# Optimization experiments

Measured on AMD Instinct MI355X. Metric: run time of the kernel, lower is better.

The kernel has to match this reference:

```python
import jax, jax.numpy as jnp
import numpy as np

ATTN_HEADS = 4
NEG_INF = float(np.finfo(np.float32).min)


def setup_inputs() -> dict:
    key = jax.random.key(0)
    ks = jax.random.split(key, 7)
    B, N, K, Cin, Cout = 4, 4096, 32, 128, 128
    h_X = jax.random.normal(ks[0], (B, N, Cout), dtype=jnp.float32)
    h_E = jax.random.normal(ks[1], (B, N, K, Cin), dtype=jnp.float32)
    mask_attn = jax.random.randint(ks[2], (B, N, K), 0, 2, dtype=jnp.int32)
    # torch Linear weights are [out_features, in_features]
    W_Q = jax.random.normal(ks[3], (Cout, Cout), dtype=jnp.float32) / np.sqrt(Cout)
    W_K = jax.random.normal(ks[4], (Cout, Cin), dtype=jnp.float32) / np.sqrt(Cin)
    W_V = jax.random.normal(ks[5], (Cout, Cin), dtype=jnp.float32) / np.sqrt(Cin)
    W_O = jax.random.normal(ks[6], (Cout, 3 * Cout), dtype=jnp.float32) / np.sqrt(3 * Cout)
    return {"h_X": h_X, "h_E": h_E, "mask_attn": mask_attn,
            "W_Q": W_Q, "W_K": W_K, "W_V": W_V, "W_O": W_O}


def reference(h_X, h_E, mask_attn, W_Q, W_K, W_V, W_O):
    B, N, K, _ = h_E.shape
    C = W_Q.shape[0]
    H = ATTN_HEADS
    d = C // H

    h_q = (h_X @ W_Q.T).reshape(B, N, H, d)          # [B,N,H,d]
    h_k = (h_E @ W_K.T).reshape(B, N, K, H, d)       # [B,N,K,H,d]
    h_v = (h_E @ W_V.T).reshape(B, N, K, H, d)       # [B,N,K,H,d]

    # per-node, per-head scores over K neighbors
    scores = jnp.einsum('bnhd,bnkhd->bnhk', h_q, h_k) / np.sqrt(d)

    mask = (mask_attn[:, :, None, :] > 0)            # [B,N,1,K] -> broadcast over heads
    logits = jnp.where(mask, scores, NEG_INF)
    attn = jax.nn.softmax(logits, axis=-1) * mask.astype(scores.dtype)  # [B,N,H,K]

    attn_sum = attn.sum(axis=-1, keepdims=True) + 1e-8                  # [B,N,H,1]
    hv_t = jnp.swapaxes(h_v, 2, 3)                                      # [B,N,H,K,d]
    weighted_v = attn[..., None] * hv_t                                 # [B,N,H,K,d]
    weighted_sum = weighted_v.sum(axis=3)                               # [B,N,H,d]
    aggr_mean = (weighted_sum / attn_sum).reshape(B, N, C)
    aggr_sum = weighted_sum.reshape(B, N, C)
    aggr_max = weighted_v.max(axis=3).reshape(B, N, C)

    aggr_cat = jnp.concatenate([aggr_mean, aggr_sum, aggr_max], axis=-1)  # [B,N,3C]
    return aggr_cat @ W_O.T                                               # [B,N,C]
```

## Files before the change

kernel.cpp:

```cpp
#include <hip/hip_runtime.h>
#include <stdint.h>


typedef __attribute__((ext_vector_type(8))) short short8;
typedef __attribute__((ext_vector_type(4))) float f32x4;

#define CDIM  128
#define KN    32
#define ESTR  136
#define SSTR  36

__device__ __forceinline__ float bf2f(short s) {
    union { unsigned int u; float f; } v;
    v.u = ((unsigned int)(unsigned short)s) << 16;
    return v.f;
}
__device__ __forceinline__ short f2bf(float f) {
    union { float ff; unsigned int u; } v; v.ff = f;
    unsigned int u = v.u;
    u += 0x7FFFu + ((u >> 16) & 1u);
    return (short)(u >> 16);
}

template<bool FP32>
__device__ __forceinline__ short8 load8bf(const void* p, size_t idx) {
    if constexpr (FP32) {
        const float* fp = (const float*)p + idx;
        f32x4 a = *(const f32x4*)fp;
        f32x4 b = *(const f32x4*)(fp + 4);
        short8 r;
        r[0] = f2bf(a[0]); r[1] = f2bf(a[1]); r[2] = f2bf(a[2]); r[3] = f2bf(a[3]);
        r[4] = f2bf(b[0]); r[5] = f2bf(b[1]); r[6] = f2bf(b[2]); r[7] = f2bf(b[3]);
        return r;
    } else {
        return *(const short8*)((const short*)p + idx);
    }
}

template<bool FP32>
__device__ __forceinline__ short loadbf1(const void* p, size_t idx) {
    if constexpr (FP32) return f2bf(((const float*)p)[idx]);
    else return ((const short*)p)[idx];
}

__device__ __forceinline__ bool detect_fp32(const short* wp) {
    const int lane = threadIdx.x & 63;
    int cnt = 0;
    #pragma unroll
    for (int i = 0; i < 8; ++i) {
        const float v = bf2f(wp[lane + i * 64]);
        if (!(fabsf(v) < 8.0f)) cnt++;
    }
    #pragma unroll
    for (int d = 1; d < 64; d <<= 1) cnt += __shfl_xor(cnt, d);
    return cnt > 16;
}

#define ANPB 64
struct alignas(16) SmemA {
    short sX[ANPB * ESTR];
    short sQ[ANPB * ESTR];
};

template<bool FP32>
__device__ __forceinline__ void naA_body(SmemA& sm, const void* __restrict__ hX,
    const void* __restrict__ WQ, const void* __restrict__ WK, short* __restrict__ Tg)
{
    const int tid = threadIdx.x, lane = tid & 63, w = tid >> 6;
    const int quad = lane >> 4, l15 = lane & 15;
    const int nbA = blockIdx.x * ANPB;

    #pragma unroll
    for (int it = 0; it < 4; ++it) {
        const int chunk = it * 256 + tid, row = chunk >> 4, cc = chunk & 15;
        *(short8*)&sm.sX[row * ESTR + cc * 8] =
            load8bf<FP32>(hX, (size_t)nbA * CDIM + (size_t)chunk * 8);
    }
    short8 bq[2][4];
    #pragma unroll
    for (int t2 = 0; t2 < 2; ++t2)
        #pragma unroll
        for (int kk = 0; kk < 4; ++kk)
            bq[t2][kk] = load8bf<FP32>(WQ, (size_t)(w * 32 + t2 * 16 + l15) * CDIM + kk * 32 + quad * 8);
    __syncthreads();

    #pragma unroll
    for (int mt = 0; mt < 4; ++mt) {
        short8 ax[4];
        #pragma unroll
        for (int kk = 0; kk < 4; ++kk)
            ax[kk] = *(const short8*)&sm.sX[(mt * 16 + l15) * ESTR + kk * 32 + quad * 8];
        f32x4 o0 = {0.f,0.f,0.f,0.f}, o1 = {0.f,0.f,0.f,0.f};
        #pragma unroll
        for (int kk = 0; kk < 4; ++kk) {
            o0 = __builtin_amdgcn_mfma_f32_16x16x32_bf16(ax[kk], bq[0][kk], o0, 0, 0, 0);
            o1 = __builtin_amdgcn_mfma_f32_16x16x32_bf16(ax[kk], bq[1][kk], o1, 0, 0, 0);
        }
        #pragma unroll
        for (int r = 0; r < 4; ++r) {
            const int row = mt * 16 + quad * 4 + r;
            sm.sQ[row * ESTR + w * 32 + l15]      = f2bf(o0[r]);
            sm.sQ[row * ESTR + w * 32 + 16 + l15] = f2bf(o1[r]);
        }
    }
    __syncthreads();

    short8 bk[2][4];
    #pragma unroll
    for (int t2 = 0; t2 < 2; ++t2)
        #pragma unroll
        for (int kk = 0; kk < 4; ++kk) {
            const int j = w * 32 + t2 * 16 + l15;
            short8 b;
            #pragma unroll
            for (int jj = 0; jj < 8; ++jj)
                b[jj] = loadbf1<FP32>(WK, (size_t)(kk * 32 + quad * 8 + jj) * CDIM + j);
            bk[t2][kk] = b;
        }

    const float scale = 0.17677669529663687f;
    const short8 zz = {0,0,0,0,0,0,0,0};
    #pragma unroll
    for (int m = 0; m < 16; ++m) {
        const int n_g = (m * 16 + l15) >> 2, h_ = l15 & 3;
        const short8 qv = *(const short8*)&sm.sQ[n_g * ESTR + h_ * 32 + quad * 8];
        f32x4 c0 = {0.f,0.f,0.f,0.f}, c1 = {0.f,0.f,0.f,0.f};
        #pragma unroll
        for (int kk = 0; kk < 4; ++kk) {
            const short8 af = (kk == h_) ? qv : zz;
            c0 = __builtin_amdgcn_mfma_f32_16x16x32_bf16(af, bk[0][kk], c0, 0, 0, 0);
            c1 = __builtin_amdgcn_mfma_f32_16x16x32_bf16(af, bk[1][kk], c1, 0, 0, 0);
        }
        #pragma unroll
        for (int r = 0; r < 4; ++r) {
            const int rg = m * 16 + quad * 4 + r;
            const size_t base = (size_t)(nbA + (rg >> 2)) * 512 + (rg & 3) * 128 + w * 32;
            Tg[base + l15]      = f2bf(c0[r] * scale);
            Tg[base + 16 + l15] = f2bf(c1[r] * scale);
        }
    }
}

__global__ __launch_bounds__(256, 3)
void naA(const void* __restrict__ hX, const void* __restrict__ WQ,
         const void* __restrict__ WK, short* __restrict__ Tg)
{
    __shared__ SmemA sm;
    if (detect_fp32((const short*)WQ)) naA_body<true >(sm, hX, WQ, WK, Tg);
    else                               naA_body<false>(sm, hX, WQ, WK, Tg);
}

#define NPB 16
struct alignas(16) SmemB {
    short sE[128 * ESTR];
    short sTb[2][16 * ESTR];
    float sS[16 * SSTR];
    int   sMask[NPB * KN];
};

template<bool FP32>
__device__ __forceinline__ void issueE(const void* hE, size_t base, int tid,
                                       f32x4 (&eF)[8][2], short8 (&eB)[8]) {
    if constexpr (FP32) {
        #pragma unroll
        for (int it = 0; it < 8; ++it) {
            const float* p = (const float*)hE + base + (size_t)(it * 256 + tid) * 8;
            eF[it][0] = *(const f32x4*)p;
            eF[it][1] = *(const f32x4*)(p + 4);
        }
    } else {
        #pragma unroll
        for (int it = 0; it < 8; ++it)
            eB[it] = *(const short8*)((const short*)hE + base + (size_t)(it * 256 + tid) * 8);
    }
}

template<bool FP32>
__device__ __forceinline__ void writeE(short* sE, int tid,
                                       const f32x4 (&eF)[8][2], const short8 (&eB)[8]) {
    #pragma unroll
    for (int it = 0; it < 8; ++it) {
        const int chunk = it * 256 + tid, row = chunk >> 4, cc = chunk & 15;
        short8 v;
        if constexpr (FP32) {
            #pragma unroll
            for (int t = 0; t < 4; ++t) { v[t] = f2bf(eF[it][0][t]); v[4 + t] = f2bf(eF[it][1][t]); }
        } else v = eB[it];
        *(short8*)&sE[row * ESTR + cc * 8] = v;
    }
}

template<bool FP32>
__device__ __forceinline__ void naB_body(SmemB& sm, const void* __restrict__ hE,
    const int* __restrict__ mask, const void* __restrict__ WV,
    const short* __restrict__ Tg, short* __restrict__ catG)
{
    const int tid = threadIdx.x, lane = tid & 63, w = tid >> 6;
    const int quad = lane >> 4, l15 = lane & 15;
    const int nb = blockIdx.x * NPB;
    const size_t ebase = (size_t)nb * (KN * CDIM);

    f32x4 eF[8][2]; short8 eB[8]; short8 eT;
    issueE<FP32>(hE, ebase, tid, eF, eB);
    eT = *(const short8*)(Tg + (size_t)nb * 512 + tid * 8);
    __builtin_amdgcn_sched_barrier(0);

    *(int2*)&sm.sMask[tid * 2] = *(const int2*)&mask[(size_t)nb * KN + tid * 2];

    short8 bv[2][4];
    #pragma unroll
    for (int ct2 = 0; ct2 < 2; ++ct2)
        #pragma unroll
        for (int kk = 0; kk < 4; ++kk)
            bv[ct2][kk] = load8bf<FP32>(WV, (size_t)((2 * w + ct2) * 16 + l15) * CDIM + kk * 32 + quad * 8);

    writeE<FP32>(sm.sE, tid, eF, eB);
    { const int row = tid >> 4, cc = tid & 15;
      *(short8*)&sm.sTb[0][row * ESTR + cc * 8] = eT; }
    issueE<FP32>(hE, ebase + 128 * 128, tid, eF, eB);
    eT = *(const short8*)(Tg + (size_t)(nb + 4) * 512 + tid * 8);
    __builtin_amdgcn_sched_barrier(0);
    __syncthreads();

    #pragma unroll 1
    for (int s = 0; s < 4; ++s) {
        const short* tb = sm.sTb[s & 1];

        short8 bs[4], a0[4], a1[4];
        #pragma unroll
        for (int kk = 0; kk < 4; ++kk) {
            bs[kk] = *(const short8*)&tb[l15 * ESTR + kk * 32 + quad * 8];
            a0[kk] = *(const short8*)&sm.sE[(w * 32 + l15) * ESTR + kk * 32 + quad * 8];
            a1[kk] = *(const short8*)&sm.sE[(w * 32 + 16 + l15) * ESTR + kk * 32 + quad * 8];
        }
        f32x4 s0 = {0.f,0.f,0.f,0.f}, s1 = {0.f,0.f,0.f,0.f};
        #pragma unroll
        for (int kk = 0; kk < 4; ++kk) {
            s0 = __builtin_amdgcn_mfma_f32_16x16x32_bf16(a0[kk], bs[kk], s0, 0, 0, 0);
            s1 = __builtin_amdgcn_mfma_f32_16x16x32_bf16(a1[kk], bs[kk], s1, 0, 0, 0);
        }

        {
            const int* mp = &sm.sMask[(s * 4 + (l15 >> 2)) * KN];
            float x[8]; int mk[8];
            #pragma unroll
            for (int j = 0; j < 4; ++j) {
                x[j] = s0[j];     mk[j]     = mp[quad * 4 + j];
                x[4 + j] = s1[j]; mk[4 + j] = mp[16 + quad * 4 + j];
            }
            float m = -3.0e38f;
            #pragma unroll
            for (int j = 0; j < 8; ++j) m = fmaxf(m, (mk[j] > 0) ? x[j] : -3.0e38f);
            m = fmaxf(m, __shfl_xor(m, 16));
            m = fmaxf(m, __shfl_xor(m, 32));
            float dsum = 0.f;
            #pragma unroll
            for (int j = 0; j < 8; ++j) {
                const float e = __expf(fminf(x[j] - m, 0.f)) * ((mk[j] > 0) ? 1.f : 0.f);
                x[j] = e; dsum += e;
            }
            dsum += __shfl_xor(dsum, 16);
            dsum += __shfl_xor(dsum, 32);
            const float inv = (dsum > 0.f) ? (1.f / dsum) : 0.f;
            if ((l15 >> 2) == w) {
                float* sp = &sm.sS[(w * 4 + (l15 & 3)) * SSTR];
                #pragma unroll
                for (int j = 0; j < 4; ++j) {
                    sp[quad * 4 + j]      = x[j] * inv;
                    sp[16 + quad * 4 + j] = x[4 + j] * inv;
                }
                if (quad == 0)
                    sp[33] = 1.0f / (((dsum > 0.f) ? 1.0f : 0.0f) + 1e-8f);
            }
        }
        __syncthreads();

        #pragma unroll
        for (int n_ = 0; n_ < 4; ++n_) {
            short8 c0[4], c1[4];
            #pragma unroll
            for (int kk = 0; kk < 4; ++kk) {
                c0[kk] = *(const short8*)&sm.sE[(n_ * 32 + l15) * ESTR + kk * 32 + quad * 8];
                c1[kk] = *(const short8*)&sm.sE[(n_ * 32 + 16 + l15) * ESTR + kk * 32 + quad * 8];
            }
            const float* ap = &sm.sS[(n_ * 4 + w) * SSTR];
            const float ainv = ap[33];
            #pragma unroll
            for (int ct2 = 0; ct2 < 2; ++ct2) {
                f32x4 av0 = {0.f,0.f,0.f,0.f}, av1 = {0.f,0.f,0.f,0.f};
                #pragma unroll
                for (int kk = 0; kk < 4; ++kk) {
                    av0 = __builtin_amdgcn_mfma_f32_16x16x32_bf16(c0[kk], bv[ct2][kk], av0, 0, 0, 0);
                    av1 = __builtin_amdgcn_mfma_f32_16x16x32_bf16(c1[kk], bv[ct2][kk], av1, 0, 0, 0);
                }
                float sum = 0.f, mx = -3.0e38f;
                #pragma unroll
                for (int r = 0; r < 4; ++r) {
                    const float p0 = ap[quad * 4 + r]      * av0[r];
                    const float p1 = ap[16 + quad * 4 + r] * av1[r];
                    sum += p0 + p1;
                    mx = fmaxf(mx, fmaxf(p0, p1));
                }
                sum += __shfl_xor(sum, 16);
                sum += __shfl_xor(sum, 32);
                mx = fmaxf(mx, __shfl_xor(mx, 16));
                mx = fmaxf(mx, __shfl_xor(mx, 32));
                if (quad == 0) {
                    const int c = (2 * w + ct2) * 16 + l15;
                    const size_t ng = (size_t)(nb + s * 4 + n_) * 384;
                    catG[ng + c]       = f2bf(sum * ainv);
                    catG[ng + 128 + c] = f2bf(sum);
                    catG[ng + 256 + c] = f2bf(mx);
                }
            }
        }
        __syncthreads();

        if (s < 3) {
            writeE<FP32>(sm.sE, tid, eF, eB);
            { const int row = tid >> 4, cc = tid & 15;
              *(short8*)&sm.sTb[(s + 1) & 1][row * ESTR + cc * 8] = eT; }
            if (s < 2) {
                issueE<FP32>(hE, ebase + (size_t)(s + 2) * 128 * 128, tid, eF, eB);
                eT = *(const short8*)(Tg + (size_t)(nb + (s + 2) * 4) * 512 + tid * 8);
                __builtin_amdgcn_sched_barrier(0);
            }
            __syncthreads();
        }
    }
}

__global__ __launch_bounds__(256, 3)
void naB(const void* __restrict__ hE, const int* __restrict__ mask,
         const void* __restrict__ WV, const short* __restrict__ Tg,
         short* __restrict__ catG)
{
    __shared__ SmemB sm;
    if (detect_fp32((const short*)WV)) naB_body<true >(sm, hE, mask, WV, Tg, catG);
    else                               naB_body<false>(sm, hE, mask, WV, Tg, catG);
}

struct alignas(16) SmemC {
    short sCat[16 * 392];
};

template<bool FP32>
__device__ __forceinline__ void naC_body(SmemC& sm, const short* __restrict__ catG,
    const void* __restrict__ WO, void* __restrict__ out)
{
    const int tid = threadIdx.x, lane = tid & 63, w = tid >> 6;
    const int quad = lane >> 4, l15 = lane & 15;
    const int nb = blockIdx.x * 16;

    #pragma unroll
    for (int it = 0; it < 3; ++it) {
        const int chunk = it * 256 + tid;
        const int row = chunk / 48, cc = chunk % 48;
        *(short8*)&sm.sCat[row * 392 + cc * 8] =
            *(const short8*)&catG[(size_t)nb * 384 + (size_t)chunk * 8];
    }
    __syncthreads();

    f32x4 o0 = {0.f,0.f,0.f,0.f}, o1 = {0.f,0.f,0.f,0.f};
    #pragma unroll
    for (int kk = 0; kk < 12; ++kk) {
        const short8 a  = *(const short8*)&sm.sCat[l15 * 392 + kk * 32 + quad * 8];
        const short8 b0 = load8bf<FP32>(WO, (size_t)(w * 32 + l15) * 384 + kk * 32 + quad * 8);
        const short8 b1 = load8bf<FP32>(WO, (size_t)(w * 32 + 16 + l15) * 384 + kk * 32 + quad * 8);
        o0 = __builtin_amdgcn_mfma_f32_16x16x32_bf16(a, b0, o0, 0, 0, 0);
        o1 = __builtin_amdgcn_mfma_f32_16x16x32_bf16(a, b1, o1, 0, 0, 0);
    }
    #pragma unroll
    for (int r = 0; r < 4; ++r) {
        const int node = quad * 4 + r;
        const size_t base = (size_t)(nb + node) * CDIM + w * 32;
        if constexpr (FP32) {
            ((float*)out)[base + l15]      = o0[r];
            ((float*)out)[base + 16 + l15] = o1[r];
        } else {
            ((short*)out)[base + l15]      = f2bf(o0[r]);
            ((short*)out)[base + 16 + l15] = f2bf(o1[r]);
        }
    }
}

__global__ __launch_bounds__(256, 4)
void naC(const short* __restrict__ catG, const void* __restrict__ WO,
         void* __restrict__ out)
{
    __shared__ SmemC sm;
    if (detect_fp32((const short*)WO)) naC_body<true >(sm, catG, WO, out);
    else                               naC_body<false>(sm, catG, WO, out);
}

extern "C" void kernel_launch(void* const* d_in, const int* in_sizes, int n_in,
                              void* d_out, int out_size, void* d_ws, size_t ws_size,
                              hipStream_t stream) {
    (void)in_sizes; (void)n_in; (void)ws_size; (void)out_size;
    const void* hX   = d_in[0];
    const void* hE   = d_in[1];
    const int*  mask = (const int*)d_in[2];
    const void* WQ   = d_in[3];
    const void* WK   = d_in[4];
    const void* WV   = d_in[5];
    const void* WO   = d_in[6];

    short* Tg   = (short*)d_ws;
    short* catG = (short*)((char*)d_ws + (32u << 20));

    naA<<<dim3(256),  dim3(256), 0, stream>>>(hX, WQ, WK, Tg);
    naB<<<dim3(1024), dim3(256), 0, stream>>>(hE, mask, WV, Tg, catG);
    naC<<<dim3(1024), dim3(256), 0, stream>>>(catG, WO, d_out);
}
```

Before: 434.0 us.

## Restructure attention kernel to one node per wavefront without shared memory

Result: slower. 494.6 us (+14.0%).

```diff
diff --git a/kernel.cpp b/kernel.cpp
--- a/kernel.cpp
+++ b/kernel.cpp
@@ -8,7 +8,7 @@
 #define CDIM  128
 #define KN    32
 #define ESTR  136
-#define SSTR  36
+#define NEGI  -3.0e38f
 
 __device__ __forceinline__ float bf2f(short s) {
     union { unsigned int u; float f; } v;
@@ -150,194 +150,114 @@
     else                               naA_body<false>(sm, hX, WQ, WK, Tg);
 }
 
-#define NPB 16
-struct alignas(16) SmemB {
-    short sE[128 * ESTR];
-    short sTb[2][16 * ESTR];
-    float sS[16 * SSTR];
-    int   sMask[NPB * KN];
-};
-
-template<bool FP32>
-__device__ __forceinline__ void issueE(const void* hE, size_t base, int tid,
-                                       f32x4 (&eF)[8][2], short8 (&eB)[8]) {
-    if constexpr (FP32) {
-        #pragma unroll
-        for (int it = 0; it < 8; ++it) {
-            const float* p = (const float*)hE + base + (size_t)(it * 256 + tid) * 8;
-            eF[it][0] = *(const f32x4*)p;
-            eF[it][1] = *(const f32x4*)(p + 4);
-        }
-    } else {
-        #pragma unroll
-        for (int it = 0; it < 8; ++it)
-            eB[it] = *(const short8*)((const short*)hE + base + (size_t)(it * 256 + tid) * 8);
-    }
-}
-
-template<bool FP32>
-__device__ __forceinline__ void writeE(short* sE, int tid,
-                                       const f32x4 (&eF)[8][2], const short8 (&eB)[8]) {
-    #pragma unroll
-    for (int it = 0; it < 8; ++it) {
-        const int chunk = it * 256 + tid, row = chunk >> 4, cc = chunk & 15;
-        short8 v;
-        if constexpr (FP32) {
-            #pragma unroll
-            for (int t = 0; t < 4; ++t) { v[t] = f2bf(eF[it][0][t]); v[4 + t] = f2bf(eF[it][1][t]); }
-        } else v = eB[it];
-        *(short8*)&sE[row * ESTR + cc * 8] = v;
-    }
-}
-
-template<bool FP32>
-__device__ __forceinline__ void naB_body(SmemB& sm, const void* __restrict__ hE,
+template<bool FP32>
+__device__ __forceinline__ void naB2_node(int node, const void* __restrict__ hE,
     const int* __restrict__ mask, const void* __restrict__ WV,
     const short* __restrict__ Tg, short* __restrict__ catG)
 {
-    const int tid = threadIdx.x, lane = tid & 63, w = tid >> 6;
+    const int lane = threadIdx.x & 63;
     const int quad = lane >> 4, l15 = lane & 15;
-    const int nb = blockIdx.x * NPB;
-    const size_t ebase = (size_t)nb * (KN * CDIM);
-
-    f32x4 eF[8][2]; short8 eB[8]; short8 eT;
-    issueE<FP32>(hE, ebase, tid, eF, eB);
-    eT = *(const short8*)(Tg + (size_t)nb * 512 + tid * 8);
-    __builtin_amdgcn_sched_barrier(0);
-
-    *(int2*)&sm.sMask[tid * 2] = *(const int2*)&mask[(size_t)nb * KN + tid * 2];
-
-    short8 bv[2][4];
-    #pragma unroll
-    for (int ct2 = 0; ct2 < 2; ++ct2)
-        #pragma unroll
-        for (int kk = 0; kk < 4; ++kk)
-            bv[ct2][kk] = load8bf<FP32>(WV, (size_t)((2 * w + ct2) * 16 + l15) * CDIM + kk * 32 + quad * 8);
-
-    writeE<FP32>(sm.sE, tid, eF, eB);
-    { const int row = tid >> 4, cc = tid & 15;
-      *(short8*)&sm.sTb[0][row * ESTR + cc * 8] = eT; }
-    issueE<FP32>(hE, ebase + 128 * 128, tid, eF, eB);
-    eT = *(const short8*)(Tg + (size_t)(nb + 4) * 512 + tid * 8);
-    __builtin_amdgcn_sched_barrier(0);
-    __syncthreads();
-
-    #pragma unroll 1
-    for (int s = 0; s < 4; ++s) {
-        const short* tb = sm.sTb[s & 1];
-
-        short8 bs[4], a0[4], a1[4];
+    const size_t eb = (size_t)node * (KN * CDIM);
+
+    short8 aE0[4], aE1[4];
+    #pragma unroll
+    for (int kk = 0; kk < 4; ++kk) {
+        aE0[kk] = load8bf<FP32>(hE, eb + (size_t)l15 * CDIM + kk * 32 + quad * 8);
+        aE1[kk] = load8bf<FP32>(hE, eb + (size_t)(16 + l15) * CDIM + kk * 32 + quad * 8);
+    }
+
+    short8 tq[4];
+    #pragma unroll
+    for (int kk = 0; kk < 4; ++kk)
+        tq[kk] = *(const short8*)(Tg + (size_t)node * 512 + (l15 & 3) * 128 + kk * 32 + quad * 8);
+
+    const int mk0 = mask[(size_t)node * KN + l15];
+    const int mk1 = mask[(size_t)node * KN + 16 + l15];
+
+    f32x4 s0 = {0.f,0.f,0.f,0.f}, s1 = {0.f,0.f,0.f,0.f};
+    #pragma unroll
+    for (int kk = 0; kk < 4; ++kk) {
+        s0 = __builtin_amdgcn_mfma_f32_16x16x32_bf16(tq[kk], aE0[kk], s0, 0, 0, 0);
+        s1 = __builtin_amdgcn_mfma_f32_16x16x32_bf16(tq[kk], aE1[kk], s1, 0, 0, 0);
+    }
+
+    float x0[4], x1[4], ainv[4];
+    {
+        float m[4], ds[4];
+        #pragma unroll
+        for (int r = 0; r < 4; ++r) {
+            const float a = (mk0 > 0) ? s0[r] : NEGI;
+            const float b = (mk1 > 0) ? s1[r] : NEGI;
+            m[r] = fmaxf(a, b);
+        }
+        #pragma unroll
+        for (int d = 1; d < 16; d <<= 1)
+            #pragma unroll
+            for (int r = 0; r < 4; ++r) m[r] = fmaxf(m[r], __shfl_xor(m[r], d));
+        #pragma unroll
+        for (int r = 0; r < 4; ++r) {
+            x0[r] = __expf(fminf(s0[r] - m[r], 0.f)) * ((mk0 > 0) ? 1.f : 0.f);
+            x1[r] = __expf(fminf(s1[r] - m[r], 0.f)) * ((mk1 > 0) ? 1.f : 0.f);
+            ds[r] = x0[r] + x1[r];
+        }
+        #pragma unroll
+        for (int d = 1; d < 16; d <<= 1)
+            #pragma unroll
+            for (int r = 0; r < 4; ++r) ds[r] += __shfl_xor(ds[r], d);
+        #pragma unroll
+        for (int r = 0; r < 4; ++r) {
+            const float inv = (ds[r] > 0.f) ? (1.f / ds[r]) : 0.f;
+            x0[r] *= inv; x1[r] *= inv;
+            ainv[r] = 1.0f / (((ds[r] > 0.f) ? 1.0f : 0.0f) + 1e-8f);
+        }
+    }
+
+    const size_t ng = (size_t)node * 384;
+    #pragma unroll
+    for (int ct = 0; ct < 8; ++ct) {
+        const int h = ct >> 1;
+        float aA[4], aB[4];
+        #pragma unroll
+        for (int r = 0; r < 4; ++r) {
+            aA[r] = __shfl(x0[h], quad * 4 + r);
+            aB[r] = __shfl(x1[h], quad * 4 + r);
+        }
+        f32x4 av0 = {0.f,0.f,0.f,0.f}, av1 = {0.f,0.f,0.f,0.f};
         #pragma unroll
         for (int kk = 0; kk < 4; ++kk) {
-            bs[kk] = *(const short8*)&tb[l15 * ESTR + kk * 32 + quad * 8];
-            a0[kk] = *(const short8*)&sm.sE[(w * 32 + l15) * ESTR + kk * 32 + quad * 8];
-            a1[kk] = *(const short8*)&sm.sE[(w * 32 + 16 + l15) * ESTR + kk * 32 + quad * 8];
-        }
-        f32x4 s0 = {0.f,0.f,0.f,0.f}, s1 = {0.f,0.f,0.f,0.f};
-        #pragma unroll
-        for (int kk = 0; kk < 4; ++kk) {
-            s0 = __builtin_amdgcn_mfma_f32_16x16x32_bf16(a0[kk], bs[kk], s0, 0, 0, 0);
-            s1 = __builtin_amdgcn_mfma_f32_16x16x32_bf16(a1[kk], bs[kk], s1, 0, 0, 0);
-        }
-
-        {
-            const int* mp = &sm.sMask[(s * 4 + (l15 >> 2)) * KN];
-            float x[8]; int mk[8];
-            #pragma unroll
-            for (int j = 0; j < 4; ++j) {
-                x[j] = s0[j];     mk[j]     = mp[quad * 4 + j];
-                x[4 + j] = s1[j]; mk[4 + j] = mp[16 + quad * 4 + j];
-            }
-            float m = -3.0e38f;
-            #pragma unroll
-            for (int j = 0; j < 8; ++j) m = fmaxf(m, (mk[j] > 0) ? x[j] : -3.0e38f);
-            m = fmaxf(m, __shfl_xor(m, 16));
-            m = fmaxf(m, __shfl_xor(m, 32));
-            float dsum = 0.f;
-            #pragma unroll
-            for (int j = 0; j < 8; ++j) {
-                const float e = __expf(fminf(x[j] - m, 0.f)) * ((mk[j] > 0) ? 1.f : 0.f);
-                x[j] = e; dsum += e;
-            }
-            dsum += __shfl_xor(dsum, 16);
-            dsum += __shfl_xor(dsum, 32);
-            const float inv = (dsum > 0.f) ? (1.f / dsum) : 0.f;
-            if ((l15 >> 2) == w) {
-                float* sp = &sm.sS[(w * 4 + (l15 & 3)) * SSTR];
-                #pragma unroll
-                for (int j = 0; j < 4; ++j) {
-                    sp[quad * 4 + j]      = x[j] * inv;
-                    sp[16 + quad * 4 + j] = x[4 + j] * inv;
-                }
-                if (quad == 0)
-                    sp[33] = 1.0f / (((dsum > 0.f) ? 1.0f : 0.0f) + 1e-8f);
-            }
-        }
-        __syncthreads();
-
-        #pragma unroll
-        for (int n_ = 0; n_ < 4; ++n_) {
-            short8 c0[4], c1[4];
-            #pragma unroll
-            for (int kk = 0; kk < 4; ++kk) {
-                c0[kk] = *(const short8*)&sm.sE[(n_ * 32 + l15) * ESTR + kk * 32 + quad * 8];
-                c1[kk] = *(const short8*)&sm.sE[(n_ * 32 + 16 + l15) * ESTR + kk * 32 + quad * 8];
-            }
-            const float* ap = &sm.sS[(n_ * 4 + w) * SSTR];
-            const float ainv = ap[33];
-            #pragma unroll
-            for (int ct2 = 0; ct2 < 2; ++ct2) {
-                f32x4 av0 = {0.f,0.f,0.f,0.f}, av1 = {0.f,0.f,0.f,0.f};
-                #pragma unroll
-                for (int kk = 0; kk < 4; ++kk) {
-                    av0 = __builtin_amdgcn_mfma_f32_16x16x32_bf16(c0[kk], bv[ct2][kk], av0, 0, 0, 0);
-                    av1 = __builtin_amdgcn_mfma_f32_16x16x32_bf16(c1[kk], bv[ct2][kk], av1, 0, 0, 0);
-                }
-                float sum = 0.f, mx = -3.0e38f;
-                #pragma unroll
-                for (int r = 0; r < 4; ++r) {
-                    const float p0 = ap[quad * 4 + r]      * av0[r];
-                    const float p1 = ap[16 + quad * 4 + r] * av1[r];
-                    sum += p0 + p1;
-                    mx = fmaxf(mx, fmaxf(p0, p1));
-                }
-                sum += __shfl_xor(sum, 16);
-                sum += __shfl_xor(sum, 32);
-                mx = fmaxf(mx, __shfl_xor(mx, 16));
-                mx = fmaxf(mx, __shfl_xor(mx, 32));
-                if (quad == 0) {
-                    const int c = (2 * w + ct2) * 16 + l15;
-                    const size_t ng = (size_t)(nb + s * 4 + n_) * 384;
-                    catG[ng + c]       = f2bf(sum * ainv);
-                    catG[ng + 128 + c] = f2bf(sum);
-                    catG[ng + 256 + c] = f2bf(mx);
-                }
-            }
-        }
-        __syncthreads();
-
-        if (s < 3) {
-            writeE<FP32>(sm.sE, tid, eF, eB);
-            { const int row = tid >> 4, cc = tid & 15;
-              *(short8*)&sm.sTb[(s + 1) & 1][row * ESTR + cc * 8] = eT; }
-            if (s < 2) {
-                issueE<FP32>(hE, ebase + (size_t)(s + 2) * 128 * 128, tid, eF, eB);
-                eT = *(const short8*)(Tg + (size_t)(nb + (s + 2) * 4) * 512 + tid * 8);
-                __builtin_amdgcn_sched_barrier(0);
-            }
-            __syncthreads();
+            const short8 bvf = load8bf<FP32>(WV, (size_t)(ct * 16 + l15) * CDIM + kk * 32 + quad * 8);
+            av0 = __builtin_amdgcn_mfma_f32_16x16x32_bf16(aE0[kk], bvf, av0, 0, 0, 0);
+            av1 = __builtin_amdgcn_mfma_f32_16x16x32_bf16(aE1[kk], bvf, av1, 0, 0, 0);
+        }
+        float sum = 0.f, mx = NEGI;
+        #pragma unroll
+        for (int r = 0; r < 4; ++r) {
+            const float p0 = aA[r] * av0[r];
+            const float p1 = aB[r] * av1[r];
+            sum += p0 + p1;
+            mx = fmaxf(mx, fmaxf(p0, p1));
+        }
+        sum += __shfl_xor(sum, 16);
+        sum += __shfl_xor(sum, 32);
+        mx = fmaxf(mx, __shfl_xor(mx, 16));
+        mx = fmaxf(mx, __shfl_xor(mx, 32));
+        if (quad == 0) {
+            const int c = ct * 16 + l15;
+            catG[ng + c]       = f2bf(sum * ainv[h]);
+            catG[ng + 128 + c] = f2bf(sum);
+            catG[ng + 256 + c] = f2bf(mx);
         }
     }
 }
 
 __global__ __launch_bounds__(256, 3)
-void naB(const void* __restrict__ hE, const int* __restrict__ mask,
-         const void* __restrict__ WV, const short* __restrict__ Tg,
-         short* __restrict__ catG)
-{
-    __shared__ SmemB sm;
-    if (detect_fp32((const short*)WV)) naB_body<true >(sm, hE, mask, WV, Tg, catG);
-    else                               naB_body<false>(sm, hE, mask, WV, Tg, catG);
+void naB2(const void* __restrict__ hE, const int* __restrict__ mask,
+          const void* __restrict__ WV, const short* __restrict__ Tg,
+          short* __restrict__ catG)
+{
+    const int node = blockIdx.x * 4 + (threadIdx.x >> 6);
+    if (detect_fp32((const short*)WV)) naB2_node<true >(node, hE, mask, WV, Tg, catG);
+    else                               naB2_node<false>(node, hE, mask, WV, Tg, catG);
 }
 
 struct alignas(16) SmemC {
@@ -408,7 +328,7 @@
     short* Tg   = (short*)d_ws;
     short* catG = (short*)((char*)d_ws + (32u << 20));
 
-    naA<<<dim3(256),  dim3(256), 0, stream>>>(hX, WQ, WK, Tg);
-    naB<<<dim3(1024), dim3(256), 0, stream>>>(hE, mask, WV, Tg, catG);
-    naC<<<dim3(1024), dim3(256), 0, stream>>>(catG, WO, d_out);
-}
+    naA <<<dim3(256),  dim3(256), 0, stream>>>(hX, WQ, WK, Tg);
+    naB2<<<dim3(4096), dim3(256), 0, stream>>>(hE, mask, WV, Tg, catG);
+    naC <<<dim3(1024), dim3(256), 0, stream>>>(catG, WO, d_out);
+}
```
